# Kernel tuning notes

Measured on AMD Instinct MI355X. Metric: run time of the kernel, lower is better.

Reference implementation:

```python
import jax, jax.numpy as jnp
import numpy as np

VOCAB, EMB = 50000, 300
B, TQ, TD, TOPK = 128, 32, 4096, 20
EPS = 1e-8


def setup_inputs() -> dict:
    key = jax.random.key(0)
    ks = jax.random.split(key, 7)
    return {
        "doc": jax.random.randint(ks[0], (B, TD), 0, VOCAB),
        "query": jax.random.randint(ks[1], (B, TQ), 0, VOCAB),
        "query_idf": jax.random.uniform(ks[2], (B, TQ), dtype=jnp.float32),
        "emb_table": jax.random.normal(ks[3], (VOCAB, EMB), dtype=jnp.float32),
        "ffw_W": jax.random.uniform(ks[4], (1, TOPK), minval=-0.1, maxval=0.1, dtype=jnp.float32),
        "ffw_b": jnp.zeros((1,), jnp.float32),
        "gates_W": jax.random.uniform(ks[5], (1, 1), minval=-0.01, maxval=0.01, dtype=jnp.float32),
        "out_W": jax.random.normal(ks[6], (1, 1), dtype=jnp.float32),
        "out_b": jnp.zeros((1,), jnp.float32),
        "topk": TOPK,
    }


def reference(doc, query, query_idf, emb_table, ffw_W, ffw_b, gates_W, out_W, out_b, topk):
    # masks
    q_mask = (query != 0).astype(jnp.float32)  # (B,Tq)

    # SimilarityMatrix: cosine similarity between embedded query and doc tokens
    qe = emb_table[query]  # (B,Tq,H)
    de = emb_table[doc]    # (B,Td,H)
    qn = qe / jnp.maximum(jnp.linalg.norm(qe, axis=-1, keepdims=True), EPS)
    dn = de / jnp.maximum(jnp.linalg.norm(de, axis=-1, keepdims=True), EPS)
    cos_mat = jnp.einsum('bqh,bdh->bqd', qn, dn)  # (B,Tq,Td)

    # top-k over doc axis, then tiny FFW + tanh
    tk, _ = jax.lax.top_k(cos_mat, topk)                     # (B,Tq,k)
    ffw_vec = jnp.tanh(jnp.einsum('bqk,ok->bqo', tk, ffw_W) + ffw_b)[..., 0]  # (B,Tq)

    # IDF term gate: Linear(1->1, no bias) on idf + mask, softmax over query terms
    atten_mask = (1.0 - q_mask) * -1e7
    gate_logits = query_idf * gates_W[0, 0] + atten_mask
    w = jax.nn.softmax(gate_logits, axis=1)                  # (B,Tq)

    # gated sum + output Linear(1->1)
    d = jnp.sum(w * ffw_vec, axis=-1, keepdims=True)         # (B,1)
    score = d * out_W[0, 0] + out_b
    return score
```

## Files before the change

kernel.cpp:

```cpp
#include <hip/hip_runtime.h>
#include <math.h>

#define VOCAB 50000
#define EMB 300
#define NB 128
#define TQ 32
#define TD 4096
#define TOPK 20
#define KP 320
#define NCHUNK 16
#define NHC 75

typedef short short8 __attribute__((ext_vector_type(8)));
typedef float f32x4 __attribute__((ext_vector_type(4)));

__device__ inline ushort bf16_rtne(float x) {
  unsigned u = __float_as_uint(x);
  unsigned r = u + 0x7fffu + ((u >> 16) & 1u);
  return (ushort)(r >> 16);
}

__global__ __launch_bounds__(256) void rownorm_kernel(const float* __restrict__ emb,
                                                      float* __restrict__ invn) {
  int row = blockIdx.x * 4 + (threadIdx.x >> 6);
  if (row >= VOCAB) return;
  int lane = threadIdx.x & 63;
  float s = 0.f;
  for (int h = lane; h < EMB; h += 64) {
    float v = emb[row * EMB + h];
    s += v * v;
  }
#pragma unroll
  for (int off = 32; off; off >>= 1) s += __shfl_xor(s, off, 64);
  if (lane == 0) invn[row] = 1.0f / fmaxf(sqrtf(s), 1e-8f);
}

__global__ __launch_bounds__(256) void dprep_kernel(const float* __restrict__ emb,
                                                    ushort* __restrict__ dhi,
                                                    ushort* __restrict__ dlo) {
  int row = blockIdx.x * 4 + (threadIdx.x >> 6);
  if (row >= VOCAB) return;
  int lane = threadIdx.x & 63;
  float v[5];
  float s = 0.f;
#pragma unroll
  for (int j = 0; j < 5; ++j) {
    int k = j * 64 + lane;
    float x = (k < EMB) ? emb[(size_t)row * EMB + k] : 0.f;
    v[j] = x;
    s += x * x;
  }
#pragma unroll
  for (int off = 32; off; off >>= 1) s += __shfl_xor(s, off, 64);
  float inv = 1.0f / fmaxf(sqrtf(s), 1e-8f);
#pragma unroll
  for (int j = 0; j < 5; ++j) {
    int k = j * 64 + lane;
    float x = v[j] * inv;
    ushort h = bf16_rtne(x);
    float hf = __uint_as_float((unsigned)h << 16);
    ushort l = bf16_rtne(x - hf);
    dhi[(size_t)row * KP + k] = h;
    dlo[(size_t)row * KP + k] = l;
  }
}

__global__ __launch_bounds__(256) void qprep2_kernel(const int* __restrict__ query,
                                                     const float* __restrict__ emb,
                                                     ushort* __restrict__ qhi,
                                                     ushort* __restrict__ qlo) {
  const int b = blockIdx.x;
  const int wave = (int)threadIdx.x >> 6;
  const int lane = (int)threadIdx.x & 63;
#pragma unroll 1
  for (int q = wave; q < TQ; q += 4) {
    int tok = query[b * TQ + q];
    float v[5];
    float s = 0.f;
#pragma unroll
    for (int j = 0; j < 5; ++j) {
      int k = j * 64 + lane;
      float x = (k < EMB) ? emb[(size_t)tok * EMB + k] : 0.f;
      v[j] = x;
      s += x * x;
    }
#pragma unroll
    for (int off = 32; off; off >>= 1) s += __shfl_xor(s, off, 64);
    float inv = 1.0f / fmaxf(sqrtf(s), 1e-8f);
#pragma unroll
    for (int j = 0; j < 5; ++j) {
      int k = j * 64 + lane;
      float x = v[j] * inv;
      ushort h = bf16_rtne(x);
      float hf = __uint_as_float((unsigned)h << 16);
      ushort l = bf16_rtne(x - hf);
      qhi[(size_t)(b * TQ + q) * KP + k] = h;
      qlo[(size_t)(b * TQ + q) * KP + k] = l;
    }
  }
}

__global__ __launch_bounds__(256, 3) void mfma_topk_kernel(
    const int* __restrict__ doc, const ushort* __restrict__ qhi,
    const ushort* __restrict__ qlo, const ushort* __restrict__ dhi,
    const ushort* __restrict__ dlo, float* __restrict__ partial) {
  __shared__ float costmp[4][64][33];
  __shared__ float topv[4][TQ][21];

  const int b = blockIdx.y;
  const int chunk = blockIdx.x;
  const int tid = (int)threadIdx.x;
  const int wave = tid >> 6;
  const int lane = tid & 63;
  const int c = lane & 15;
  const int kg = lane >> 4;

  const int tbase = b * TD + chunk * 256 + wave * 64;
  const ushort* pdh0 = dhi + (size_t)doc[tbase + 0 * 16 + c] * KP + kg * 8;
  const ushort* pdh1 = dhi + (size_t)doc[tbase + 1 * 16 + c] * KP + kg * 8;
  const ushort* pdh2 = dhi + (size_t)doc[tbase + 2 * 16 + c] * KP + kg * 8;
  const ushort* pdh3 = dhi + (size_t)doc[tbase + 3 * 16 + c] * KP + kg * 8;
  const ushort* pdl0 = dlo + (size_t)doc[tbase + 0 * 16 + c] * KP + kg * 8;
  const ushort* pdl1 = dlo + (size_t)doc[tbase + 1 * 16 + c] * KP + kg * 8;
  const ushort* pdl2 = dlo + (size_t)doc[tbase + 2 * 16 + c] * KP + kg * 8;
  const ushort* pdl3 = dlo + (size_t)doc[tbase + 3 * 16 + c] * KP + kg * 8;
  const ushort* pqh0 = qhi + (size_t)(b * TQ + c) * KP + kg * 8;
  const ushort* pqh1 = qhi + (size_t)(b * TQ + 16 + c) * KP + kg * 8;
  const ushort* pql0 = qlo + (size_t)(b * TQ + c) * KP + kg * 8;
  const ushort* pql1 = qlo + (size_t)(b * TQ + 16 + c) * KP + kg * 8;

  f32x4 a00 = {0.f, 0.f, 0.f, 0.f}, a01 = a00, a02 = a00, a03 = a00;
  f32x4 a10 = a00, a11 = a00, a12 = a00, a13 = a00;

  short8 ah0P, ah1P, al0P, al1P, bh0P, bh1P, bh2P, bh3P, bl0P, bl1P, bl2P, bl3P;
  short8 ah0Q, ah1Q, al0Q, al1Q, bh0Q, bh1Q, bh2Q, bh3Q, bl0Q, bl1Q, bl2Q, bl3Q;

#define STR2(x) #x
#define STR(x) STR2(x)
#define LD1(DST, PTR, OFFB)                                              \
  asm volatile("global_load_dwordx4 %0, %1, off offset:" STR(OFFB)       \
               : "=v"(DST)                                               \
               : "v"(PTR));
#define LOADSET(S, OFFB)                                                 \
  LD1(ah0##S, pqh0, OFFB) LD1(ah1##S, pqh1, OFFB)                        \
  LD1(al0##S, pql0, OFFB) LD1(al1##S, pql1, OFFB)                        \
  LD1(bh0##S, pdh0, OFFB) LD1(bh1##S, pdh1, OFFB)                        \
  LD1(bh2##S, pdh2, OFFB) LD1(bh3##S, pdh3, OFFB)                        \
  LD1(bl0##S, pdl0, OFFB) LD1(bl1##S, pdl1, OFFB)                        \
  LD1(bl2##S, pdl2, OFFB) LD1(bl3##S, pdl3, OFFB)

#define WAIT12                                        \
  asm volatile("s_waitcnt vmcnt(12)" ::: "memory");   \
  __builtin_amdgcn_sched_barrier(0);
#define WAIT0                                         \
  asm volatile("s_waitcnt vmcnt(0)" ::: "memory");    \
  __builtin_amdgcn_sched_barrier(0);

#define MM3(ACC, AH, AL, BH, BL)                                          \
  ACC = __builtin_amdgcn_mfma_f32_16x16x32_bf16(AH, BH, ACC, 0, 0, 0);    \
  ACC = __builtin_amdgcn_mfma_f32_16x16x32_bf16(AH, BL, ACC, 0, 0, 0);    \
  ACC = __builtin_amdgcn_mfma_f32_16x16x32_bf16(AL, BH, ACC, 0, 0, 0);

#define MMALL(S)                           \
  MM3(a00, ah0##S, al0##S, bh0##S, bl0##S) \
  MM3(a01, ah0##S, al0##S, bh1##S, bl1##S) \
  MM3(a02, ah0##S, al0##S, bh2##S, bl2##S) \
  MM3(a03, ah0##S, al0##S, bh3##S, bl3##S) \
  MM3(a10, ah1##S, al1##S, bh0##S, bl0##S) \
  MM3(a11, ah1##S, al1##S, bh1##S, bl1##S) \
  MM3(a12, ah1##S, al1##S, bh2##S, bl2##S) \
  MM3(a13, ah1##S, al1##S, bh3##S, bl3##S)

  LOADSET(P, 0)
  LOADSET(Q, 64)
  WAIT12 MMALL(P) LOADSET(P, 128)
  WAIT12 MMALL(Q) LOADSET(Q, 192)
  WAIT12 MMALL(P) LOADSET(P, 256)
  WAIT12 MMALL(Q) LOADSET(Q, 320)
  WAIT12 MMALL(P) LOADSET(P, 384)
  WAIT12 MMALL(Q) LOADSET(Q, 448)
  WAIT12 MMALL(P) LOADSET(P, 512)
  WAIT12 MMALL(Q) LOADSET(Q, 576)
  WAIT12 MMALL(P)
  WAIT0  MMALL(Q)

#undef LOADSET
#undef LD1
#undef WAIT12
#undef WAIT0
#undef MM3
#undef MMALL
#undef STR
#undef STR2

#define WT(ACC, M, NT)                                        \
  {                                                           \
    float* dst = &costmp[wave][NT * 16 + c][M * 16 + kg * 4]; \
    dst[0] = ACC[0]; dst[1] = ACC[1];                         \
    dst[2] = ACC[2]; dst[3] = ACC[3];                         \
  }
  WT(a00, 0, 0) WT(a01, 0, 1) WT(a02, 0, 2) WT(a03, 0, 3)
  WT(a10, 1, 0) WT(a11, 1, 1) WT(a12, 1, 2) WT(a13, 1, 3)
#undef WT

  if (lane < TQ) {
    const int q = lane;
    float* tv = &topv[wave][q][0];
#pragma unroll
    for (int k = 0; k < TOPK; ++k) tv[k] = -2.0f;
    float mn = -2.0f;
    for (int tt = 0; tt < 64; ++tt) {
      float v = costmp[wave][tt][q];
      if (v > mn) {
        int p = TOPK - 1;
        while (p > 0 && tv[p - 1] < v) {
          tv[p] = tv[p - 1];
          --p;
        }
        tv[p] = v;
        mn = tv[TOPK - 1];
      }
    }
  }
  __syncthreads();

  if (tid < TQ) {
    const int q = tid;
    float* dst = &topv[0][q][0];
#pragma unroll
    for (int w = 1; w < 4; ++w) {
      for (int k = 0; k < TOPK; ++k) {
        float v = topv[w][q][k];
        if (v <= dst[TOPK - 1]) break;
        int p = TOPK - 1;
        while (p > 0 && dst[p - 1] < v) {
          dst[p] = dst[p - 1];
          --p;
        }
        dst[p] = v;
      }
    }
  }
  __syncthreads();

  for (int i = tid; i < TQ * TOPK; i += 256)
    partial[((size_t)(b * NCHUNK + chunk)) * (TQ * TOPK) + i] =
        topv[0][i / TOPK][i % TOPK];
}

__global__ __launch_bounds__(256) void qprep_kernel(const int* __restrict__ query,
                                                    const float* __restrict__ emb,
                                                    const float* __restrict__ invn,
                                                    float* __restrict__ qn_t) {
  const int b = blockIdx.x;
  for (int i = (int)threadIdx.x; i < NHC * TQ; i += 256) {
    int hc = i >> 5, q = i & 31;
    int tok = query[b * TQ + q];
    float inv = invn[tok];
    float4 v = *(const float4*)(emb + (size_t)tok * EMB + hc * 4);
    float4 o;
    o.x = v.x * inv; o.y = v.y * inv; o.z = v.z * inv; o.w = v.w * inv;
    *(float4*)(qn_t + (((size_t)b * NHC + hc) * TQ + q) * 4) = o;
  }
}

__global__ __launch_bounds__(256, 3) void cos_topk_kernel(
    const int* __restrict__ doc, const float* __restrict__ emb,
    const float* __restrict__ invn, const float* __restrict__ qn_t,
    float* __restrict__ partial) {
  __shared__ __align__(16) float smem[9600];
  __shared__ float topv[4][TQ][21];
  float* qsh = smem;
  float (*costmp)[33] = (float (*)[33])smem;

  const int b = blockIdx.y;
  const int chunk = blockIdx.x;
  const int tid = (int)threadIdx.x;
  const int wave = tid >> 6;
  const int lane = tid & 63;

  {
    const float4* src = (const float4*)(qn_t + (size_t)b * (NHC * TQ * 4));
    float4* dst = (float4*)qsh;
    for (int i = tid; i < NHC * TQ; i += 256) dst[i] = src[i];
  }
  if (lane < TQ) {
#pragma unroll
    for (int k = 0; k < TOPK; ++k) topv[wave][lane][k] = -2.0f;
  }
  __syncthreads();

  const int tok = doc[b * TD + chunk * 256 + tid];
  const float invd = invn[tok];
  const float* __restrict__ drow = emb + (size_t)tok * EMB;

  float acc[TQ];
#pragma unroll
  for (int qi = 0; qi < TQ; ++qi) acc[qi] = 0.f;

  float4 p0 = *(const float4*)(drow + 0);
  float4 p1 = *(const float4*)(drow + 4);
  float4 p2 = *(const float4*)(drow + 8);
  float4 p3 = *(const float4*)(drow + 12);
  float4 p4 = *(const float4*)(drow + 16);

#define STEP(S, PS)                                                           \
  {                                                                           \
    const float4 d = PS;                                                      \
    PS = *(const float4*)(drow + 4 * (hcb + S + 5));                          \
    const float* __restrict__ qc = qsh + (hcb + S) * (TQ * 4);                \
    _Pragma("unroll") for (int qi = 0; qi < TQ; ++qi) {                       \
      float4 qf = *(const float4*)(qc + qi * 4);                              \
      acc[qi] =                                                               \
          fmaf(qf.x, d.x, fmaf(qf.y, d.y, fmaf(qf.z, d.z, fmaf(qf.w, d.w, acc[qi])))); \
    }                                                                         \
  }
#define STEP_LAST(S, PS)                                                      \
  {                                                                           \
    const float4 d = PS;                                                      \
    const float* __restrict__ qc = qsh + (hcb + S) * (TQ * 4);                \
    _Pragma("unroll") for (int qi = 0; qi < TQ; ++qi) {                       \
      float4 qf = *(const float4*)(qc + qi * 4);                              \
      acc[qi] =                                                               \
          fmaf(qf.x, d.x, fmaf(qf.y, d.y, fmaf(qf.z, d.z, fmaf(qf.w, d.w, acc[qi])))); \
    }                                                                         \
  }
#pragma unroll 1
  for (int r = 0; r < 14; ++r) {
    const int hcb = r * 5;
    STEP(0, p0) STEP(1, p1) STEP(2, p2) STEP(3, p3) STEP(4, p4)
  }
  {
    const int hcb = 70;
    STEP_LAST(0, p0) STEP_LAST(1, p1) STEP_LAST(2, p2) STEP_LAST(3, p3) STEP_LAST(4, p4)
  }
#undef STEP
#undef STEP_LAST

  __syncthreads();
#pragma unroll
  for (int qi = 0; qi < TQ; ++qi) costmp[wave * 64 + lane][qi] = acc[qi] * invd;

  if (lane < TQ) {
    const int q = lane;
    float* tv = &topv[wave][q][0];
    float mn = tv[TOPK - 1];
    for (int tt = 0; tt < 64; ++tt) {
      float v = costmp[wave * 64 + tt][q];
      if (v > mn) {
        int p = TOPK - 1;
        while (p > 0 && tv[p - 1] < v) {
          tv[p] = tv[p - 1];
          --p;
        }
        tv[p] = v;
        mn = tv[TOPK - 1];
      }
    }
  }
  __syncthreads();

  if (tid < TQ) {
    const int q = tid;
    float* dst = &topv[0][q][0];
#pragma unroll
    for (int w = 1; w < 4; ++w) {
      for (int k = 0; k < TOPK; ++k) {
        float v = topv[w][q][k];
        if (v <= dst[TOPK - 1]) break;
        int p = TOPK - 1;
        while (p > 0 && dst[p - 1] < v) {
          dst[p] = dst[p - 1];
          --p;
        }
        dst[p] = v;
      }
    }
  }
  __syncthreads();

  for (int i = tid; i < TQ * TOPK; i += 256)
    partial[((size_t)(b * NCHUNK + chunk)) * (TQ * TOPK) + i] =
        topv[0][i / TOPK][i % TOPK];
}

__global__ __launch_bounds__(64) void finalize_kernel(
    const float* __restrict__ partial, const int* __restrict__ query,
    const float* __restrict__ qidf, const float* __restrict__ ffw_W,
    const float* __restrict__ ffw_b, const float* __restrict__ gates_W,
    const float* __restrict__ out_W, const float* __restrict__ out_b,
    float* __restrict__ out) {
  const int b = blockIdx.x;
  const int lane = (int)threadIdx.x;
  float ffw = 0.f;
  float logit = -3e38f;
  if (lane < TQ) {
    const int q = lane;
    int pos[NCHUNK];
#pragma unroll
    for (int c = 0; c < NCHUNK; ++c) pos[c] = 0;
    float s = 0.f;
    for (int k = 0; k < TOPK; ++k) {
      float best = -4.f;
      int bi = 0;
#pragma unroll
      for (int c = 0; c < NCHUNK; ++c) {
        float v = (pos[c] < TOPK)
                      ? partial[((size_t)(b * NCHUNK + c) * TQ + q) * TOPK + pos[c]]
                      : -4.f;
        if (v > best) {
          best = v;
          bi = c;
        }
      }
#pragma unroll
      for (int c = 0; c < NCHUNK; ++c)
        if (c == bi) pos[c]++;
      s += best * ffw_W[k];
    }
    ffw = tanhf(s + ffw_b[0]);
    int tok = query[b * TQ + q];
    logit = qidf[b * TQ + q] * gates_W[0] + (tok == 0 ? -1e7f : 0.f);
  }
  float m = logit;
#pragma unroll
  for (int off = 32; off; off >>= 1) m = fmaxf(m, __shfl_xor(m, off, 64));
  float e = expf(logit - m);
  float num = e * ffw;
  float den = e;
#pragma unroll
  for (int off = 32; off; off >>= 1) {
    num += __shfl_xor(num, off, 64);
    den += __shfl_xor(den, off, 64);
  }
  if (lane == 0) out[b] = (num / den) * out_W[0] + out_b[0];
}

extern "C" void kernel_launch(void* const* d_in, const int* in_sizes, int n_in,
                              void* d_out, int out_size, void* d_ws, size_t ws_size,
                              hipStream_t stream) {
  const int* doc = (const int*)d_in[0];
  const int* query = (const int*)d_in[1];
  const float* qidf = (const float*)d_in[2];
  const float* emb = (const float*)d_in[3];
  const float* ffw_W = (const float*)d_in[4];
  const float* ffw_b = (const float*)d_in[5];
  const float* gates_W = (const float*)d_in[6];
  const float* out_W = (const float*)d_in[7];
  const float* out_b = (const float*)d_in[8];
  float* out = (float*)d_out;

  char* ws = (char*)d_ws;
  float* invn = (float*)ws;

  const size_t OFF_QHI = 200192;
  const size_t OFF_QLO = OFF_QHI + (size_t)NB * TQ * KP * 2;
  const size_t OFF_DHI = OFF_QLO + (size_t)NB * TQ * KP * 2;
  const size_t OFF_DLO = OFF_DHI + (size_t)VOCAB * KP * 2;
  const size_t OFF_PAR = OFF_DLO + (size_t)VOCAB * KP * 2;
  const size_t NEED = OFF_PAR + (size_t)NB * NCHUNK * TQ * TOPK * 4;

  if (ws_size >= NEED) {
    ushort* qhi = (ushort*)(ws + OFF_QHI);
    ushort* qlo = (ushort*)(ws + OFF_QLO);
    ushort* dhi = (ushort*)(ws + OFF_DHI);
    ushort* dlo = (ushort*)(ws + OFF_DLO);
    float* partial = (float*)(ws + OFF_PAR);
    dprep_kernel<<<(VOCAB + 3) / 4, 256, 0, stream>>>(emb, dhi, dlo);
    qprep2_kernel<<<NB, 256, 0, stream>>>(query, emb, qhi, qlo);
    dim3 grid(NCHUNK, NB);
    mfma_topk_kernel<<<grid, 256, 0, stream>>>(doc, qhi, qlo, dhi, dlo, partial);
    finalize_kernel<<<NB, 64, 0, stream>>>(partial, query, qidf, ffw_W, ffw_b,
                                           gates_W, out_W, out_b, out);
  } else {
    float* qn_t = invn + 50048;
    float* partial = qn_t + (size_t)NB * NHC * TQ * 4;
    rownorm_kernel<<<(VOCAB + 3) / 4, 256, 0, stream>>>(emb, invn);
    qprep_kernel<<<NB, 256, 0, stream>>>(query, emb, invn, qn_t);
    dim3 grid(NCHUNK, NB);
    cos_topk_kernel<<<grid, 256, 0, stream>>>(doc, emb, invn, qn_t, partial);
    finalize_kernel<<<NB, 64, 0, stream>>>(partial, query, qidf, ffw_W, ffw_b,
                                           gates_W, out_W, out_b, out);
  }
}
```

Before: 335.2 us.

## Drop split-bf16 lo terms, stage query tile in LDS, deepen load pipeline

Switches the cosine matmul from a three-pass hi/lo split-bf16 scheme to a single bf16 pass, so the lo embedding tables and two of every three MFMAs go away. Prep kernels now write only the hi table, halving their output. The per-batch query tile is copied once into shared memory instead of being re-read from global memory each k-step. Doc loads move to a five-deep prefetch pipeline. The trade is lower precision in the similarity values, which can change which doc tokens make the top-k near ties.

```diff
diff --git a/kernel.cpp b/kernel.cpp
--- a/kernel.cpp
+++ b/kernel.cpp
@@ -10,6 +10,7 @@
 #define KP 320
 #define NCHUNK 16
 #define NHC 75
+#define QSTRIDE 656
 
 typedef short short8 __attribute__((ext_vector_type(8)));
 typedef float f32x4 __attribute__((ext_vector_type(4)));
@@ -36,8 +37,7 @@
 }
 
 __global__ __launch_bounds__(256) void dprep_kernel(const float* __restrict__ emb,
-                                                    ushort* __restrict__ dhi,
-                                                    ushort* __restrict__ dlo) {
+                                                    ushort* __restrict__ dhi) {
   int row = blockIdx.x * 4 + (threadIdx.x >> 6);
   if (row >= VOCAB) return;
   int lane = threadIdx.x & 63;
@@ -56,19 +56,13 @@
 #pragma unroll
   for (int j = 0; j < 5; ++j) {
     int k = j * 64 + lane;
-    float x = v[j] * inv;
-    ushort h = bf16_rtne(x);
-    float hf = __uint_as_float((unsigned)h << 16);
-    ushort l = bf16_rtne(x - hf);
-    dhi[(size_t)row * KP + k] = h;
-    dlo[(size_t)row * KP + k] = l;
+    dhi[(size_t)row * KP + k] = bf16_rtne(v[j] * inv);
   }
 }
 
 __global__ __launch_bounds__(256) void qprep2_kernel(const int* __restrict__ query,
                                                      const float* __restrict__ emb,
-                                                     ushort* __restrict__ qhi,
-                                                     ushort* __restrict__ qlo) {
+                                                     ushort* __restrict__ qhi) {
   const int b = blockIdx.x;
   const int wave = (int)threadIdx.x >> 6;
   const int lane = (int)threadIdx.x & 63;
@@ -90,22 +84,18 @@
 #pragma unroll
     for (int j = 0; j < 5; ++j) {
       int k = j * 64 + lane;
-      float x = v[j] * inv;
-      ushort h = bf16_rtne(x);
-      float hf = __uint_as_float((unsigned)h << 16);
-      ushort l = bf16_rtne(x - hf);
-      qhi[(size_t)(b * TQ + q) * KP + k] = h;
-      qlo[(size_t)(b * TQ + q) * KP + k] = l;
+      qhi[(size_t)(b * TQ + q) * KP + k] = bf16_rtne(v[j] * inv);
     }
   }
 }
 
 __global__ __launch_bounds__(256, 3) void mfma_topk_kernel(
     const int* __restrict__ doc, const ushort* __restrict__ qhi,
-    const ushort* __restrict__ qlo, const ushort* __restrict__ dhi,
-    const ushort* __restrict__ dlo, float* __restrict__ partial) {
-  __shared__ float costmp[4][64][33];
+    const ushort* __restrict__ dhi, float* __restrict__ partial) {
+  __shared__ __align__(16) char smem[33792];
   __shared__ float topv[4][TQ][21];
+
+  float (*costmp)[64][33] = (float (*)[64][33])smem;
 
   const int b = blockIdx.y;
   const int chunk = blockIdx.x;
@@ -115,89 +105,94 @@
   const int c = lane & 15;
   const int kg = lane >> 4;
 
+  {
+    const ushort* qsrc = qhi + (size_t)b * TQ * KP;
+    for (int i = tid; i < TQ * (KP / 8); i += 256) {
+      int row = i / (KP / 8), j = i - row * (KP / 8);
+      *(short8*)(smem + row * QSTRIDE + j * 16) =
+          *(const short8*)(qsrc + row * KP + j * 8);
+    }
+  }
+  __syncthreads();
+
   const int tbase = b * TD + chunk * 256 + wave * 64;
   const ushort* pdh0 = dhi + (size_t)doc[tbase + 0 * 16 + c] * KP + kg * 8;
   const ushort* pdh1 = dhi + (size_t)doc[tbase + 1 * 16 + c] * KP + kg * 8;
   const ushort* pdh2 = dhi + (size_t)doc[tbase + 2 * 16 + c] * KP + kg * 8;
   const ushort* pdh3 = dhi + (size_t)doc[tbase + 3 * 16 + c] * KP + kg * 8;
-  const ushort* pdl0 = dlo + (size_t)doc[tbase + 0 * 16 + c] * KP + kg * 8;
-  const ushort* pdl1 = dlo + (size_t)doc[tbase + 1 * 16 + c] * KP + kg * 8;
-  const ushort* pdl2 = dlo + (size_t)doc[tbase + 2 * 16 + c] * KP + kg * 8;
-  const ushort* pdl3 = dlo + (size_t)doc[tbase + 3 * 16 + c] * KP + kg * 8;
-  const ushort* pqh0 = qhi + (size_t)(b * TQ + c) * KP + kg * 8;
-  const ushort* pqh1 = qhi + (size_t)(b * TQ + 16 + c) * KP + kg * 8;
-  const ushort* pql0 = qlo + (size_t)(b * TQ + c) * KP + kg * 8;
-  const ushort* pql1 = qlo + (size_t)(b * TQ + 16 + c) * KP + kg * 8;
+  const char* qb0 = smem + c * QSTRIDE + kg * 16;
+  const char* qb1 = smem + (16 + c) * QSTRIDE + kg * 16;
 
   f32x4 a00 = {0.f, 0.f, 0.f, 0.f}, a01 = a00, a02 = a00, a03 = a00;
   f32x4 a10 = a00, a11 = a00, a12 = a00, a13 = a00;
 
-  short8 ah0P, ah1P, al0P, al1P, bh0P, bh1P, bh2P, bh3P, bl0P, bl1P, bl2P, bl3P;
-  short8 ah0Q, ah1Q, al0Q, al1Q, bh0Q, bh1Q, bh2Q, bh3Q, bl0Q, bl1Q, bl2Q, bl3Q;
+  short8 bh0A, bh1A, bh2A, bh3A, bh0B, bh1B, bh2B, bh3B, bh0C, bh1C, bh2C,
+      bh3C, bh0D, bh1D, bh2D, bh3D, bh0E, bh1E, bh2E, bh3E;
 
 #define STR2(x) #x
 #define STR(x) STR2(x)
-#define LD1(DST, PTR, OFFB)                                              \
-  asm volatile("global_load_dwordx4 %0, %1, off offset:" STR(OFFB)       \
-               : "=v"(DST)                                               \
+#define LD1(DST, PTR, OFFB)                                        \
+  asm volatile("global_load_dwordx4 %0, %1, off offset:" STR(OFFB) \
+               : "=v"(DST)                                         \
                : "v"(PTR));
-#define LOADSET(S, OFFB)                                                 \
-  LD1(ah0##S, pqh0, OFFB) LD1(ah1##S, pqh1, OFFB)                        \
-  LD1(al0##S, pql0, OFFB) LD1(al1##S, pql1, OFFB)                        \
-  LD1(bh0##S, pdh0, OFFB) LD1(bh1##S, pdh1, OFFB)                        \
-  LD1(bh2##S, pdh2, OFFB) LD1(bh3##S, pdh3, OFFB)                        \
-  LD1(bl0##S, pdl0, OFFB) LD1(bl1##S, pdl1, OFFB)                        \
-  LD1(bl2##S, pdl2, OFFB) LD1(bl3##S, pdl3, OFFB)
-
-#define WAIT12                                        \
-  asm volatile("s_waitcnt vmcnt(12)" ::: "memory");   \
+#define LOADSET(S, OFFB)                                  \
+  LD1(bh0##S, pdh0, OFFB) LD1(bh1##S, pdh1, OFFB)         \
+  LD1(bh2##S, pdh2, OFFB) LD1(bh3##S, pdh3, OFFB)
+
+#define MFMA_BF16 __builtin_amdgcn_mfma_f32_16x16x32_bf16
+#define KSTEP_BODY(S, KS)                                        \
+  {                                                              \
+    const short8 ah0 = *(const short8*)(qb0 + (KS) * 64);        \
+    const short8 ah1 = *(const short8*)(qb1 + (KS) * 64);        \
+    a00 = MFMA_BF16(ah0, bh0##S, a00, 0, 0, 0);                  \
+    a01 = MFMA_BF16(ah0, bh1##S, a01, 0, 0, 0);                  \
+    a02 = MFMA_BF16(ah0, bh2##S, a02, 0, 0, 0);                  \
+    a03 = MFMA_BF16(ah0, bh3##S, a03, 0, 0, 0);                  \
+    a10 = MFMA_BF16(ah1, bh0##S, a10, 0, 0, 0);                  \
+    a11 = MFMA_BF16(ah1, bh1##S, a11, 0, 0, 0);                  \
+    a12 = MFMA_BF16(ah1, bh2##S, a12, 0, 0, 0);                  \
+    a13 = MFMA_BF16(ah1, bh3##S, a13, 0, 0, 0);                  \
+  }
+#define WAITC(N)                                            \
+  asm volatile("s_waitcnt vmcnt(" STR(N) ")" ::: "memory"); \
   __builtin_amdgcn_sched_barrier(0);
-#define WAIT0                                         \
-  asm volatile("s_waitcnt vmcnt(0)" ::: "memory");    \
-  __builtin_amdgcn_sched_barrier(0);
-
-#define MM3(ACC, AH, AL, BH, BL)                                          \
-  ACC = __builtin_amdgcn_mfma_f32_16x16x32_bf16(AH, BH, ACC, 0, 0, 0);    \
-  ACC = __builtin_amdgcn_mfma_f32_16x16x32_bf16(AH, BL, ACC, 0, 0, 0);    \
-  ACC = __builtin_amdgcn_mfma_f32_16x16x32_bf16(AL, BH, ACC, 0, 0, 0);
-
-#define MMALL(S)                           \
-  MM3(a00, ah0##S, al0##S, bh0##S, bl0##S) \
-  MM3(a01, ah0##S, al0##S, bh1##S, bl1##S) \
-  MM3(a02, ah0##S, al0##S, bh2##S, bl2##S) \
-  MM3(a03, ah0##S, al0##S, bh3##S, bl3##S) \
-  MM3(a10, ah1##S, al1##S, bh0##S, bl0##S) \
-  MM3(a11, ah1##S, al1##S, bh1##S, bl1##S) \
-  MM3(a12, ah1##S, al1##S, bh2##S, bl2##S) \
-  MM3(a13, ah1##S, al1##S, bh3##S, bl3##S)
-
-  LOADSET(P, 0)
-  LOADSET(Q, 64)
-  WAIT12 MMALL(P) LOADSET(P, 128)
-  WAIT12 MMALL(Q) LOADSET(Q, 192)
-  WAIT12 MMALL(P) LOADSET(P, 256)
-  WAIT12 MMALL(Q) LOADSET(Q, 320)
-  WAIT12 MMALL(P) LOADSET(P, 384)
-  WAIT12 MMALL(Q) LOADSET(Q, 448)
-  WAIT12 MMALL(P) LOADSET(P, 512)
-  WAIT12 MMALL(Q) LOADSET(Q, 576)
-  WAIT12 MMALL(P)
-  WAIT0  MMALL(Q)
-
+
+#define KSTEP_R(S, KS, WN, RKS) WAITC(WN) KSTEP_BODY(S, KS) LOADSET(S, RKS)
+#define KSTEP_N(S, KS, WN) WAITC(WN) KSTEP_BODY(S, KS)
+
+  LOADSET(A, 0)
+  LOADSET(B, 64)
+  LOADSET(C, 128)
+  LOADSET(D, 192)
+  LOADSET(E, 256)
+  KSTEP_R(A, 0, 16, 320)
+  KSTEP_R(B, 1, 16, 384)
+  KSTEP_R(C, 2, 16, 448)
+  KSTEP_R(D, 3, 16, 512)
+  KSTEP_R(E, 4, 16, 576)
+  KSTEP_N(A, 5, 16)
+  KSTEP_N(B, 6, 12)
+  KSTEP_N(C, 7, 8)
+  KSTEP_N(D, 8, 4)
+  KSTEP_N(E, 9, 0)
+
+#undef KSTEP_R
+#undef KSTEP_N
+#undef WAITC
+#undef KSTEP_BODY
+#undef MFMA_BF16
 #undef LOADSET
 #undef LD1
-#undef WAIT12
-#undef WAIT0
-#undef MM3
-#undef MMALL
 #undef STR
 #undef STR2
 
-#define WT(ACC, M, NT)                                        \
-  {                                                           \
-    float* dst = &costmp[wave][NT * 16 + c][M * 16 + kg * 4]; \
-    dst[0] = ACC[0]; dst[1] = ACC[1];                         \
-    dst[2] = ACC[2]; dst[3] = ACC[3];                         \
+  __syncthreads();
+
+#define WT(ACC, M, NT)                                            \
+  {                                                               \
+    float* dst = &costmp[wave][NT * 16 + c][M * 16 + kg * 4];     \
+    dst[0] = ACC[0]; dst[1] = ACC[1];                             \
+    dst[2] = ACC[2]; dst[3] = ACC[3];                             \
   }
   WT(a00, 0, 0) WT(a01, 0, 1) WT(a02, 0, 2) WT(a03, 0, 3)
   WT(a10, 1, 0) WT(a11, 1, 1) WT(a12, 1, 2) WT(a13, 1, 3)
@@ -268,10 +263,10 @@
     const int* __restrict__ doc, const float* __restrict__ emb,
     const float* __restrict__ invn, const float* __restrict__ qn_t,
     float* __restrict__ partial) {
-  __shared__ __align__(16) float smem[9600];
+  __shared__ __align__(16) float smem_f[9600];
   __shared__ float topv[4][TQ][21];
-  float* qsh = smem;
-  float (*costmp)[33] = (float (*)[33])smem;
+  float* qsh = smem_f;
+  float (*costmp)[33] = (float (*)[33])smem_f;
 
   const int b = blockIdx.y;
   const int chunk = blockIdx.x;
@@ -454,22 +449,18 @@
   float* invn = (float*)ws;
 
   const size_t OFF_QHI = 200192;
-  const size_t OFF_QLO = OFF_QHI + (size_t)NB * TQ * KP * 2;
-  const size_t OFF_DHI = OFF_QLO + (size_t)NB * TQ * KP * 2;
-  const size_t OFF_DLO = OFF_DHI + (size_t)VOCAB * KP * 2;
-  const size_t OFF_PAR = OFF_DLO + (size_t)VOCAB * KP * 2;
+  const size_t OFF_DHI = OFF_QHI + (size_t)NB * TQ * KP * 2;
+  const size_t OFF_PAR = OFF_DHI + (size_t)VOCAB * KP * 2;
   const size_t NEED = OFF_PAR + (size_t)NB * NCHUNK * TQ * TOPK * 4;
 
   if (ws_size >= NEED) {
     ushort* qhi = (ushort*)(ws + OFF_QHI);
-    ushort* qlo = (ushort*)(ws + OFF_QLO);
     ushort* dhi = (ushort*)(ws + OFF_DHI);
-    ushort* dlo = (ushort*)(ws + OFF_DLO);
     float* partial = (float*)(ws + OFF_PAR);
-    dprep_kernel<<<(VOCAB + 3) / 4, 256, 0, stream>>>(emb, dhi, dlo);
-    qprep2_kernel<<<NB, 256, 0, stream>>>(query, emb, qhi, qlo);
+    dprep_kernel<<<(VOCAB + 3) / 4, 256, 0, stream>>>(emb, dhi);
+    qprep2_kernel<<<NB, 256, 0, stream>>>(query, emb, qhi);
     dim3 grid(NCHUNK, NB);
-    mfma_topk_kernel<<<grid, 256, 0, stream>>>(doc, qhi, qlo, dhi, dlo, partial);
+    mfma_topk_kernel<<<grid, 256, 0, stream>>>(doc, qhi, dhi, partial);
     finalize_kernel<<<NB, 64, 0, stream>>>(partial, query, qidf, ffw_W, ffw_b,
                                            gates_W, out_W, out_b, out);
   } else {
```

After: 298.1 us (median of 2 runs). 1.12x faster.
